# Optimization experiments

Hardware: AMD Instinct MI355X
Metric: run time of the kernel (lower is better)

The kernel has to match this reference:

```python
import jax, jax.numpy as jnp
import numpy as np

B, T = 16, 2048
V, E, H, C = 32000, 512, 4, 3  # vocab, embed, heads, context (history 2 + current)
EPS = 1e-5


def setup_inputs() -> dict:
    key = jax.random.key(0)
    k0, k1, k2, k3, k4, k5, k6 = jax.random.split(key, 7)
    tokens = jax.random.randint(k0, (B, T), 0, V)
    embed_table = jax.random.normal(k1, (V, E), dtype=jnp.float32)
    pos = jax.random.normal(k2, (H, E, C), dtype=jnp.float32) * (1.0 / np.sqrt(H))
    ffn_w = jax.random.normal(k3, (E, E), dtype=jnp.float32) * (1.0 / np.sqrt(E))
    ffn_b = jax.random.normal(k4, (E,), dtype=jnp.float32) * 0.01
    ln_g = jnp.ones((E,), dtype=jnp.float32)
    ln_b = jnp.zeros((E,), dtype=jnp.float32)
    return {"tokens": tokens, "embed_table": embed_table, "pos": pos,
            "ffn_w": ffn_w, "ffn_b": ffn_b, "ln_g": ln_g, "ln_b": ln_b}


def reference(tokens, embed_table, pos, ffn_w, ffn_b, ln_g, ln_b):
    # embed lookup: [B, T, E]
    x = embed_table[tokens]
    # prepend zero history, extract sliding windows of size C: [B, T, C, E]
    x_cat = jnp.concatenate([jnp.zeros((B, C - 1, E), dtype=x.dtype), x], axis=1)
    x_win = jnp.stack([x_cat[:, i:i + T] for i in range(C)], axis=2)
    # multi-head positional scores: pos viewed as [H, C, E]
    pos_hce = jnp.transpose(pos, (0, 2, 1))  # [H, C, E]
    w = jnp.einsum('btce,hce->bthc', x_win, pos_hce)          # scores
    out = jnp.einsum('bthc,btce->bte', w, x_win) / (H * C)    # weighted sum
    # FFN (torch Linear: y = x @ W^T + b)
    out = out @ ffn_w.T + ffn_b
    # LayerNorm
    mu = jnp.mean(out, axis=-1, keepdims=True)
    var = jnp.mean(jnp.square(out - mu), axis=-1, keepdims=True)
    out = (out - mu) * jax.lax.rsqrt(var + EPS) * ln_g + ln_b
    # swish
    return out * jax.nn.sigmoid(out)
```

## Files before the change

kernel.cpp:

```cpp
#include <hip/hip_runtime.h>
#include <hip/hip_bf16.h>


#define Bq 16
#define Tq 2048
#define Eq 512
#define Cq 3
#define Hq 4
#define Mq (Bq * Tq)
#define LN_EPS 1e-5f

typedef __attribute__((ext_vector_type(8))) short bf16x8;
typedef __attribute__((ext_vector_type(4))) float f32x4;
typedef __attribute__((ext_vector_type(8))) unsigned short u16x8;

__device__ __forceinline__ unsigned short f2bf(float f) {
    unsigned int u = __float_as_uint(f);
    u += 0x7fffu + ((u >> 16) & 1u);
    return (unsigned short)(u >> 16);
}

__global__ void prep_kernel(const float* __restrict__ pos,
                            const float* __restrict__ ffn_w,
                            float* __restrict__ Pt,
                            unsigned short* __restrict__ Wb) {
    int i = blockIdx.x * blockDim.x + threadIdx.x;
    if (i < Cq * Eq) {
        int c = i / Eq, e = i % Eq;
        float s = 0.f;
#pragma unroll
        for (int h = 0; h < Hq; ++h) s += pos[(h * Eq + e) * Cq + c];
        Pt[i] = s;
    }
    int nth = blockDim.x * gridDim.x;
    for (int j = i; j < Eq * Eq; j += nth) Wb[j] = f2bf(ffn_w[j]);
}

__global__ __launch_bounds__(256) void ctx_kernel(const int* __restrict__ tokens,
                                                  const float* __restrict__ tbl,
                                                  const float* __restrict__ Pt,
                                                  unsigned short* __restrict__ out1) {
    const int wave = threadIdx.x >> 6;
    const int lane = threadIdx.x & 63;
    const int tt = blockIdx.x * 4 + wave;
    const int b = tt >> 11;
    const int t = tt & (Tq - 1);

    float x[Cq][8];
    float s[Cq];
#pragma unroll
    for (int c = 0; c < Cq; ++c) {
        const int r = t - (Cq - 1) + c;
        if (r >= 0) {
            const int tok = tokens[(b << 11) + r];
            const float4* row = reinterpret_cast<const float4*>(tbl + (long)tok * Eq + lane * 8);
            float4 v0 = row[0], v1 = row[1];
            x[c][0] = v0.x; x[c][1] = v0.y; x[c][2] = v0.z; x[c][3] = v0.w;
            x[c][4] = v1.x; x[c][5] = v1.y; x[c][6] = v1.z; x[c][7] = v1.w;
        } else {
#pragma unroll
            for (int j = 0; j < 8; ++j) x[c][j] = 0.f;
        }
        const float4* pp = reinterpret_cast<const float4*>(Pt + c * Eq + lane * 8);
        float4 p0 = pp[0], p1 = pp[1];
        s[c] = x[c][0] * p0.x + x[c][1] * p0.y + x[c][2] * p0.z + x[c][3] * p0.w
             + x[c][4] * p1.x + x[c][5] * p1.y + x[c][6] * p1.z + x[c][7] * p1.w;
    }
#pragma unroll
    for (int m = 1; m < 64; m <<= 1) {
        s[0] += __shfl_xor(s[0], m, 64);
        s[1] += __shfl_xor(s[1], m, 64);
        s[2] += __shfl_xor(s[2], m, 64);
    }
    const float inv = 1.f / (Hq * Cq);
    u16x8 o;
#pragma unroll
    for (int j = 0; j < 8; ++j) {
        float v = (s[0] * x[0][j] + s[1] * x[1][j] + s[2] * x[2][j]) * inv;
        o[j] = f2bf(v);
    }
    *reinterpret_cast<u16x8*>(out1 + (long)tt * Eq + lane * 8) = o;
}

__global__ __launch_bounds__(512, 4) void ffn_ln_kernel(const unsigned short* __restrict__ A,
                                                        const unsigned short* __restrict__ Wb,
                                                        const float* __restrict__ bias,
                                                        const float* __restrict__ ln_g,
                                                        const float* __restrict__ ln_b,
                                                        float* __restrict__ out) {
    __shared__ __align__(16) char Atile[2][8192];
    __shared__ float lds_sum[64][8];
    __shared__ float lds_sq[64][8];
    __shared__ float lds_mu[64];
    __shared__ float lds_rs[64];

    const int tid = threadIdx.x;
    const int wave = tid >> 6;
    const int lane = tid & 63;
    const int lr = lane & 15;
    const int lg = lane >> 4;
    const int m0 = blockIdx.x << 6;
    const int n0 = wave << 6;

    const char* Ap = reinterpret_cast<const char*>(A) + (long)m0 * (Eq * 2);
    const short* Bp = reinterpret_cast<const short*>(Wb) + (long)n0 * Eq;

    const int r_st = tid >> 3;
    const int cb0 = (((tid & 7) ^ (r_st & 7)) << 4);
    const char* Asrc_base = Ap + r_st * 1024 + cb0;
    char* lds_wave_base[2];
    lds_wave_base[0] = &Atile[0][wave * 1024];
    lds_wave_base[1] = &Atile[1][wave * 1024];

    f32x4 acc[4][4];
#pragma unroll
    for (int i = 0; i < 4; ++i)
#pragma unroll
        for (int j = 0; j < 4; ++j) acc[i][j] = (f32x4){0.f, 0.f, 0.f, 0.f};

    __builtin_amdgcn_global_load_lds(
        (const __attribute__((address_space(1))) void*)(Asrc_base),
        (__attribute__((address_space(3))) void*)(lds_wave_base[0]), 16, 0, 0);
    __syncthreads();

    int buf = 0;
#pragma unroll
    for (int kb = 0; kb < 8; ++kb) {
        if (kb < 7) {
            __builtin_amdgcn_global_load_lds(
                (const __attribute__((address_space(1))) void*)(Asrc_base + (kb + 1) * 128),
                (__attribute__((address_space(3))) void*)(lds_wave_base[buf ^ 1]), 16, 0, 0);
        }
#pragma unroll
        for (int ks = 0; ks < 2; ++ks) {
            bf16x8 afrag[4], bfrag[4];
#pragma unroll
            for (int mf = 0; mf < 4; ++mf) {
                const int r = mf * 16 + lr;
                const int phys = r * 128 + ((ks * 64 + lg * 16) ^ ((r & 7) << 4));
                afrag[mf] = *reinterpret_cast<const bf16x8*>(&Atile[buf][phys]);
            }
#pragma unroll
            for (int nf = 0; nf < 4; ++nf)
                bfrag[nf] = *reinterpret_cast<const bf16x8*>(Bp + (nf * 16 + lr) * Eq + kb * 64 + ks * 32 + lg * 8);
#pragma unroll
            for (int mf = 0; mf < 4; ++mf)
#pragma unroll
                for (int nf = 0; nf < 4; ++nf)
                    acc[mf][nf] = __builtin_amdgcn_mfma_f32_16x16x32_bf16(afrag[mf], bfrag[nf], acc[mf][nf], 0, 0, 0);
        }
        __syncthreads();
        buf ^= 1;
    }

    float bcol[4];
#pragma unroll
    for (int nf = 0; nf < 4; ++nf) bcol[nf] = bias[n0 + nf * 16 + lr];

#pragma unroll
    for (int mf = 0; mf < 4; ++mf) {
#pragma unroll
        for (int i = 0; i < 4; ++i) {
            float sm = 0.f, sq = 0.f;
#pragma unroll
            for (int nf = 0; nf < 4; ++nf) {
                float v = acc[mf][nf][i] + bcol[nf];
                acc[mf][nf][i] = v;
                sm += v;
                sq += v * v;
            }
#pragma unroll
            for (int msk = 1; msk < 16; msk <<= 1) {
                sm += __shfl_xor(sm, msk, 64);
                sq += __shfl_xor(sq, msk, 64);
            }
            if (lr == 0) {
                const int row = mf * 16 + lg * 4 + i;
                lds_sum[row][wave] = sm;
                lds_sq[row][wave] = sq;
            }
        }
    }
    __syncthreads();
    if (tid < 64) {
        float sm = 0.f, sq = 0.f;
#pragma unroll
        for (int w = 0; w < 8; ++w) { sm += lds_sum[tid][w]; sq += lds_sq[tid][w]; }
        const float mu = sm * (1.f / Eq);
        const float var = sq * (1.f / Eq) - mu * mu;
        lds_mu[tid] = mu;
        lds_rs[tid] = rsqrtf(var + LN_EPS);
    }
    __syncthreads();

    float gcol[4], bbcol[4];
#pragma unroll
    for (int nf = 0; nf < 4; ++nf) {
        gcol[nf] = ln_g[n0 + nf * 16 + lr];
        bbcol[nf] = ln_b[n0 + nf * 16 + lr];
    }
#pragma unroll
    for (int mf = 0; mf < 4; ++mf) {
#pragma unroll
        for (int i = 0; i < 4; ++i) {
            const int row = mf * 16 + lg * 4 + i;
            const float mu = lds_mu[row];
            const float rs = lds_rs[row];
#pragma unroll
            for (int nf = 0; nf < 4; ++nf) {
                float v = acc[mf][nf][i];
                float o = (v - mu) * rs * gcol[nf] + bbcol[nf];
                o = o / (1.f + __expf(-o));
                out[(long)(m0 + row) * Eq + (n0 + nf * 16 + lr)] = o;
            }
        }
    }
}

extern "C" void kernel_launch(void* const* d_in, const int* in_sizes, int n_in,
                              void* d_out, int out_size, void* d_ws, size_t ws_size,
                              hipStream_t stream) {
    const int* tokens = (const int*)d_in[0];
    const float* tbl = (const float*)d_in[1];
    const float* pos = (const float*)d_in[2];
    const float* ffn_w = (const float*)d_in[3];
    const float* ffn_b = (const float*)d_in[4];
    const float* ln_g = (const float*)d_in[5];
    const float* ln_b = (const float*)d_in[6];
    float* out = (float*)d_out;

    char* ws = (char*)d_ws;
    float* Pt = (float*)ws;
    unsigned short* Wb = (unsigned short*)(ws + 8192);
    unsigned short* out1 = (unsigned short*)(ws + (1 << 20));

    hipLaunchKernelGGL(prep_kernel, dim3(64), dim3(256), 0, stream, pos, ffn_w, Pt, Wb);
    hipLaunchKernelGGL(ctx_kernel, dim3(Mq / 4), dim3(256), 0, stream, tokens, tbl, Pt, out1);
    hipLaunchKernelGGL(ffn_ln_kernel, dim3(Mq / 64), dim3(512), 0, stream, out1, Wb, ffn_b, ln_g, ln_b, out);
}
```

Before: 81.71 us.

## Fuse context-window gather into FFN+LayerNorm kernel with full LDS A tile

Merges the embedding gather and context-weighting kernel into the GEMM+LayerNorm kernel. Each wave gathers 10 embedding rows, reusing each across three windows instead of loading every row three times, and writes the bf16 activation row straight into a 64KB swizzled LDS tile. This removes the bf16 intermediate round-trip through global memory and one launch. The price is 64KB of LDS per block, which lowers occupancy below the declared launch bounds, plus a gather phase that no longer overlaps the MFMA loop. Embeddings are now rounded to bf16 before the weighted sum, a small precision change.

```diff
diff --git a/kernel.cpp b/kernel.cpp
--- a/kernel.cpp
+++ b/kernel.cpp
@@ -18,6 +18,9 @@
     unsigned int u = __float_as_uint(f);
     u += 0x7fffu + ((u >> 16) & 1u);
     return (unsigned short)(u >> 16);
+}
+__device__ __forceinline__ float bf2f(unsigned short h) {
+    return __uint_as_float(((unsigned int)h) << 16);
 }
 
 __global__ void prep_kernel(const float* __restrict__ pos,
@@ -36,59 +39,15 @@
     for (int j = i; j < Eq * Eq; j += nth) Wb[j] = f2bf(ffn_w[j]);
 }
 
-__global__ __launch_bounds__(256) void ctx_kernel(const int* __restrict__ tokens,
-                                                  const float* __restrict__ tbl,
-                                                  const float* __restrict__ Pt,
-                                                  unsigned short* __restrict__ out1) {
-    const int wave = threadIdx.x >> 6;
-    const int lane = threadIdx.x & 63;
-    const int tt = blockIdx.x * 4 + wave;
-    const int b = tt >> 11;
-    const int t = tt & (Tq - 1);
-
-    float x[Cq][8];
-    float s[Cq];
-#pragma unroll
-    for (int c = 0; c < Cq; ++c) {
-        const int r = t - (Cq - 1) + c;
-        if (r >= 0) {
-            const int tok = tokens[(b << 11) + r];
-            const float4* row = reinterpret_cast<const float4*>(tbl + (long)tok * Eq + lane * 8);
-            float4 v0 = row[0], v1 = row[1];
-            x[c][0] = v0.x; x[c][1] = v0.y; x[c][2] = v0.z; x[c][3] = v0.w;
-            x[c][4] = v1.x; x[c][5] = v1.y; x[c][6] = v1.z; x[c][7] = v1.w;
-        } else {
-#pragma unroll
-            for (int j = 0; j < 8; ++j) x[c][j] = 0.f;
-        }
-        const float4* pp = reinterpret_cast<const float4*>(Pt + c * Eq + lane * 8);
-        float4 p0 = pp[0], p1 = pp[1];
-        s[c] = x[c][0] * p0.x + x[c][1] * p0.y + x[c][2] * p0.z + x[c][3] * p0.w
-             + x[c][4] * p1.x + x[c][5] * p1.y + x[c][6] * p1.z + x[c][7] * p1.w;
-    }
-#pragma unroll
-    for (int m = 1; m < 64; m <<= 1) {
-        s[0] += __shfl_xor(s[0], m, 64);
-        s[1] += __shfl_xor(s[1], m, 64);
-        s[2] += __shfl_xor(s[2], m, 64);
-    }
-    const float inv = 1.f / (Hq * Cq);
-    u16x8 o;
-#pragma unroll
-    for (int j = 0; j < 8; ++j) {
-        float v = (s[0] * x[0][j] + s[1] * x[1][j] + s[2] * x[2][j]) * inv;
-        o[j] = f2bf(v);
-    }
-    *reinterpret_cast<u16x8*>(out1 + (long)tt * Eq + lane * 8) = o;
-}
-
-__global__ __launch_bounds__(512, 4) void ffn_ln_kernel(const unsigned short* __restrict__ A,
-                                                        const unsigned short* __restrict__ Wb,
-                                                        const float* __restrict__ bias,
-                                                        const float* __restrict__ ln_g,
-                                                        const float* __restrict__ ln_b,
-                                                        float* __restrict__ out) {
-    __shared__ __align__(16) char Atile[2][8192];
+__global__ __launch_bounds__(512, 4) void fused_kernel(const int* __restrict__ tokens,
+                                                       const float* __restrict__ tbl,
+                                                       const float* __restrict__ Pt,
+                                                       const unsigned short* __restrict__ Wb,
+                                                       const float* __restrict__ bias,
+                                                       const float* __restrict__ ln_g,
+                                                       const float* __restrict__ ln_b,
+                                                       float* __restrict__ out) {
+    __shared__ __align__(16) unsigned short Atile[64 * 512];
     __shared__ float lds_sum[64][8];
     __shared__ float lds_sq[64][8];
     __shared__ float lds_mu[64];
@@ -100,57 +59,95 @@
     const int lr = lane & 15;
     const int lg = lane >> 4;
     const int m0 = blockIdx.x << 6;
+    const int b = m0 >> 11;
+    const int t0w = (m0 & (Tq - 1)) + (wave << 3);
+
+    float4 pA[Cq], pB[Cq];
+#pragma unroll
+    for (int c = 0; c < Cq; ++c) {
+        const float4* pp = reinterpret_cast<const float4*>(Pt + c * Eq + lane * 8);
+        pA[c] = pp[0]; pB[c] = pp[1];
+    }
+
+    u16x8 xb[10];
+    float d[10][Cq];
+    const int tbase = b << 11;
+#pragma unroll
+    for (int li = 0; li < 10; ++li) {
+        const int t = t0w - 2 + li;
+        float4 v0 = {0.f, 0.f, 0.f, 0.f}, v1 = {0.f, 0.f, 0.f, 0.f};
+        if (t >= 0) {
+            const int tok = tokens[tbase + t];
+            const float4* rp = reinterpret_cast<const float4*>(tbl + (long)tok * Eq + lane * 8);
+            v0 = rp[0]; v1 = rp[1];
+        }
+#pragma unroll
+        for (int c = 0; c < Cq; ++c) {
+            d[li][c] = v0.x * pA[c].x + v0.y * pA[c].y + v0.z * pA[c].z + v0.w * pA[c].w
+                     + v1.x * pB[c].x + v1.y * pB[c].y + v1.z * pB[c].z + v1.w * pB[c].w;
+        }
+        u16x8 xv;
+        xv[0] = f2bf(v0.x); xv[1] = f2bf(v0.y); xv[2] = f2bf(v0.z); xv[3] = f2bf(v0.w);
+        xv[4] = f2bf(v1.x); xv[5] = f2bf(v1.y); xv[6] = f2bf(v1.z); xv[7] = f2bf(v1.w);
+        xb[li] = xv;
+    }
+#pragma unroll
+    for (int li = 0; li < 10; ++li) {
+#pragma unroll
+        for (int c = 0; c < Cq; ++c) {
+            if (li >= c && li - c <= 7) {
+#pragma unroll
+                for (int m = 1; m < 64; m <<= 1) d[li][c] += __shfl_xor(d[li][c], m, 64);
+            }
+        }
+    }
+    const float inv = 1.f / (Hq * Cq);
+#pragma unroll
+    for (int j = 0; j < 8; ++j) {
+        const float s0 = d[j][0] * inv, s1 = d[j + 1][1] * inv, s2 = d[j + 2][2] * inv;
+        u16x8 o;
+#pragma unroll
+        for (int e = 0; e < 8; ++e) {
+            const float a = s0 * bf2f((unsigned short)xb[j][e])
+                          + s1 * bf2f((unsigned short)xb[j + 1][e])
+                          + s2 * bf2f((unsigned short)xb[j + 2][e]);
+            o[e] = f2bf(a);
+        }
+        const int row = (wave << 3) + j;
+        const int phys = row * 1024 + ((lane * 16) ^ ((row & 7) << 4));
+        *reinterpret_cast<u16x8*>(reinterpret_cast<char*>(Atile) + phys) = o;
+    }
+    __syncthreads();
+
     const int n0 = wave << 6;
-
-    const char* Ap = reinterpret_cast<const char*>(A) + (long)m0 * (Eq * 2);
     const short* Bp = reinterpret_cast<const short*>(Wb) + (long)n0 * Eq;
 
-    const int r_st = tid >> 3;
-    const int cb0 = (((tid & 7) ^ (r_st & 7)) << 4);
-    const char* Asrc_base = Ap + r_st * 1024 + cb0;
-    char* lds_wave_base[2];
-    lds_wave_base[0] = &Atile[0][wave * 1024];
-    lds_wave_base[1] = &Atile[1][wave * 1024];
-
     f32x4 acc[4][4];
 #pragma unroll
     for (int i = 0; i < 4; ++i)
 #pragma unroll
         for (int j = 0; j < 4; ++j) acc[i][j] = (f32x4){0.f, 0.f, 0.f, 0.f};
 
-    __builtin_amdgcn_global_load_lds(
-        (const __attribute__((address_space(1))) void*)(Asrc_base),
-        (__attribute__((address_space(3))) void*)(lds_wave_base[0]), 16, 0, 0);
-    __syncthreads();
-
-    int buf = 0;
 #pragma unroll
     for (int kb = 0; kb < 8; ++kb) {
-        if (kb < 7) {
-            __builtin_amdgcn_global_load_lds(
-                (const __attribute__((address_space(1))) void*)(Asrc_base + (kb + 1) * 128),
-                (__attribute__((address_space(3))) void*)(lds_wave_base[buf ^ 1]), 16, 0, 0);
-        }
 #pragma unroll
         for (int ks = 0; ks < 2; ++ks) {
-            bf16x8 afrag[4], bfrag[4];
+            bf16x8 af[4], bfv[4];
 #pragma unroll
             for (int mf = 0; mf < 4; ++mf) {
                 const int r = mf * 16 + lr;
-                const int phys = r * 128 + ((ks * 64 + lg * 16) ^ ((r & 7) << 4));
-                afrag[mf] = *reinterpret_cast<const bf16x8*>(&Atile[buf][phys]);
+                const int phys = r * 1024 + ((kb * 128 + ks * 64 + lg * 16) ^ ((r & 7) << 4));
+                af[mf] = *reinterpret_cast<const bf16x8*>(reinterpret_cast<const char*>(Atile) + phys);
             }
 #pragma unroll
             for (int nf = 0; nf < 4; ++nf)
-                bfrag[nf] = *reinterpret_cast<const bf16x8*>(Bp + (nf * 16 + lr) * Eq + kb * 64 + ks * 32 + lg * 8);
+                bfv[nf] = *reinterpret_cast<const bf16x8*>(Bp + (nf * 16 + lr) * Eq + kb * 64 + ks * 32 + lg * 8);
 #pragma unroll
             for (int mf = 0; mf < 4; ++mf)
 #pragma unroll
                 for (int nf = 0; nf < 4; ++nf)
-                    acc[mf][nf] = __builtin_amdgcn_mfma_f32_16x16x32_bf16(afrag[mf], bfrag[nf], acc[mf][nf], 0, 0, 0);
-        }
-        __syncthreads();
-        buf ^= 1;
+                    acc[mf][nf] = __builtin_amdgcn_mfma_f32_16x16x32_bf16(af[mf], bfv[nf], acc[mf][nf], 0, 0, 0);
+        }
     }
 
     float bcol[4];
@@ -232,9 +229,8 @@
     char* ws = (char*)d_ws;
     float* Pt = (float*)ws;
     unsigned short* Wb = (unsigned short*)(ws + 8192);
-    unsigned short* out1 = (unsigned short*)(ws + (1 << 20));
 
     hipLaunchKernelGGL(prep_kernel, dim3(64), dim3(256), 0, stream, pos, ffn_w, Pt, Wb);
-    hipLaunchKernelGGL(ctx_kernel, dim3(Mq / 4), dim3(256), 0, stream, tokens, tbl, Pt, out1);
-    hipLaunchKernelGGL(ffn_ln_kernel, dim3(Mq / 64), dim3(512), 0, stream, out1, Wb, ffn_b, ln_g, ln_b, out);
-}
+    hipLaunchKernelGGL(fused_kernel, dim3(Mq / 64), dim3(512), 0, stream,
+                       tokens, tbl, Pt, Wb, ffn_b, ln_g, ln_b, out);
+}
```

Measured after the change: 74.80 us. -8.5%, faster.

## Pre-swizzle intermediate layout and stage full A tile plus pipelined W in LDS

Applied to the files above, without the earlier changes.

The context kernel now writes its bf16 output directly in a per-64-row swizzled tile layout, using packed hardware bf16 conversion. The FFN kernel loads the whole 64x512 A tile into LDS at once and streams per-wave W slices through a double-buffered LDS pipeline with explicit waitcnt. Previously W fragments were read straight from global memory. This is meant to cut global-load latency on W and to drop the per-step block barriers, at the cost of 128KB+ of LDS, which forces lower occupancy (launch bounds 2).

```diff
diff --git a/kernel.cpp b/kernel.cpp
--- a/kernel.cpp
+++ b/kernel.cpp
@@ -12,12 +12,19 @@
 
 typedef __attribute__((ext_vector_type(8))) short bf16x8;
 typedef __attribute__((ext_vector_type(4))) float f32x4;
-typedef __attribute__((ext_vector_type(8))) unsigned short u16x8;
-
+
+__device__ __forceinline__ unsigned int cvt_pk_bf16(float lo, float hi) {
+    unsigned int r;
+    asm("v_cvt_pk_bf16_f32 %0, %1, %2" : "=v"(r) : "v"(lo), "v"(hi));
+    return r;
+}
 __device__ __forceinline__ unsigned short f2bf(float f) {
     unsigned int u = __float_as_uint(f);
     u += 0x7fffu + ((u >> 16) & 1u);
     return (unsigned short)(u >> 16);
+}
+__device__ __forceinline__ int xaddr(int row, int kbyte) {
+    return row * 1024 + (kbyte ^ ((row & 7) << 4));
 }
 
 __global__ void prep_kernel(const float* __restrict__ pos,
@@ -39,7 +46,7 @@
 __global__ __launch_bounds__(256) void ctx_kernel(const int* __restrict__ tokens,
                                                   const float* __restrict__ tbl,
                                                   const float* __restrict__ Pt,
-                                                  unsigned short* __restrict__ out1) {
+                                                  char* __restrict__ out1) {
     const int wave = threadIdx.x >> 6;
     const int lane = threadIdx.x & 63;
     const int tt = blockIdx.x * 4 + wave;
@@ -73,24 +80,29 @@
         s[2] += __shfl_xor(s[2], m, 64);
     }
     const float inv = 1.f / (Hq * Cq);
-    u16x8 o;
-#pragma unroll
-    for (int j = 0; j < 8; ++j) {
-        float v = (s[0] * x[0][j] + s[1] * x[1][j] + s[2] * x[2][j]) * inv;
-        o[j] = f2bf(v);
-    }
-    *reinterpret_cast<u16x8*>(out1 + (long)tt * Eq + lane * 8) = o;
-}
-
-__global__ __launch_bounds__(512, 4) void ffn_ln_kernel(const unsigned short* __restrict__ A,
-                                                        const unsigned short* __restrict__ Wb,
-                                                        const float* __restrict__ bias,
-                                                        const float* __restrict__ ln_g,
-                                                        const float* __restrict__ ln_b,
-                                                        float* __restrict__ out) {
-    __shared__ __align__(16) char Atile[2][8192];
-    __shared__ float lds_sum[64][8];
-    __shared__ float lds_sq[64][8];
+    float a[8];
+#pragma unroll
+    for (int j = 0; j < 8; ++j)
+        a[j] = (s[0] * x[0][j] + s[1] * x[1][j] + s[2] * x[2][j]) * inv;
+    uint4 o;
+    o.x = cvt_pk_bf16(a[0], a[1]);
+    o.y = cvt_pk_bf16(a[2], a[3]);
+    o.z = cvt_pk_bf16(a[4], a[5]);
+    o.w = cvt_pk_bf16(a[6], a[7]);
+    char* dst = out1 + ((long)(tt >> 6) << 16) + xaddr(tt & 63, lane * 16);
+    *reinterpret_cast<uint4*>(dst) = o;
+}
+
+__global__ __launch_bounds__(512, 2) void ffn_kernel(const char* __restrict__ A1,
+                                                     const unsigned short* __restrict__ Wb,
+                                                     const float* __restrict__ bias,
+                                                     const float* __restrict__ ln_g,
+                                                     const float* __restrict__ ln_b,
+                                                     float* __restrict__ out) {
+    __shared__ __align__(16) char Alds[65536];
+    __shared__ __align__(16) char Blds[65536];
+    __shared__ float Sm[64][8];
+    __shared__ float Sq[64][8];
     __shared__ float lds_mu[64];
     __shared__ float lds_rs[64];
 
@@ -102,15 +114,33 @@
     const int m0 = blockIdx.x << 6;
     const int n0 = wave << 6;
 
-    const char* Ap = reinterpret_cast<const char*>(A) + (long)m0 * (Eq * 2);
-    const short* Bp = reinterpret_cast<const short*>(Wb) + (long)n0 * Eq;
-
-    const int r_st = tid >> 3;
-    const int cb0 = (((tid & 7) ^ (r_st & 7)) << 4);
-    const char* Asrc_base = Ap + r_st * 1024 + cb0;
-    char* lds_wave_base[2];
-    lds_wave_base[0] = &Atile[0][wave * 1024];
-    lds_wave_base[1] = &Atile[1][wave * 1024];
+    const char* Asrc = A1 + ((long)blockIdx.x << 16);
+    const char* WbB = reinterpret_cast<const char*>(Wb);
+    char* Bw = Blds + wave * 8192;
+
+    const int rn_base = lane >> 2;
+    const int s_slot = lane & 3;
+
+#pragma unroll
+    for (int q = 0; q < 8; ++q) {
+        __builtin_amdgcn_global_load_lds(
+            (const __attribute__((address_space(1))) void*)(Asrc + wave * 8192 + q * 1024 + lane * 16),
+            (__attribute__((address_space(3))) void*)(Alds + wave * 8192 + q * 1024), 16, 0, 0);
+    }
+#pragma unroll
+    for (int kc0 = 0; kc0 < 2; ++kc0) {
+#pragma unroll
+        for (int q = 0; q < 4; ++q) {
+            const int rn = q * 16 + rn_base;
+            const int n = n0 + rn;
+            const int gb = n * 1024 + kc0 * 64 + ((s_slot * 16) ^ ((n & 3) << 4));
+            __builtin_amdgcn_global_load_lds(
+                (const __attribute__((address_space(1))) void*)(WbB + gb),
+                (__attribute__((address_space(3))) void*)(Bw + kc0 * 4096 + q * 1024), 16, 0, 0);
+        }
+    }
+    asm volatile("s_waitcnt vmcnt(8)" ::: "memory");
+    __syncthreads();
 
     f32x4 acc[4][4];
 #pragma unroll
@@ -118,39 +148,38 @@
 #pragma unroll
         for (int j = 0; j < 4; ++j) acc[i][j] = (f32x4){0.f, 0.f, 0.f, 0.f};
 
-    __builtin_amdgcn_global_load_lds(
-        (const __attribute__((address_space(1))) void*)(Asrc_base),
-        (__attribute__((address_space(3))) void*)(lds_wave_base[0]), 16, 0, 0);
-    __syncthreads();
-
-    int buf = 0;
-#pragma unroll
-    for (int kb = 0; kb < 8; ++kb) {
-        if (kb < 7) {
-            __builtin_amdgcn_global_load_lds(
-                (const __attribute__((address_space(1))) void*)(Asrc_base + (kb + 1) * 128),
-                (__attribute__((address_space(3))) void*)(lds_wave_base[buf ^ 1]), 16, 0, 0);
-        }
-#pragma unroll
-        for (int ks = 0; ks < 2; ++ks) {
-            bf16x8 afrag[4], bfrag[4];
-#pragma unroll
-            for (int mf = 0; mf < 4; ++mf) {
-                const int r = mf * 16 + lr;
-                const int phys = r * 128 + ((ks * 64 + lg * 16) ^ ((r & 7) << 4));
-                afrag[mf] = *reinterpret_cast<const bf16x8*>(&Atile[buf][phys]);
-            }
+#pragma unroll
+    for (int kc = 0; kc < 16; ++kc) {
+        const int buf = (kc & 1) * 4096;
+        bf16x8 af[4], bfv[4];
+#pragma unroll
+        for (int mf = 0; mf < 4; ++mf)
+            af[mf] = *reinterpret_cast<const bf16x8*>(Alds + xaddr(mf * 16 + lr, kc * 64 + lg * 16));
+#pragma unroll
+        for (int nf = 0; nf < 4; ++nf) {
+            const int rn = nf * 16 + lr;
+            bfv[nf] = *reinterpret_cast<const bf16x8*>(Bw + buf + rn * 64 + ((lg * 16) ^ ((rn & 3) << 4)));
+        }
+        if (kc < 14) {
+            asm volatile("s_waitcnt lgkmcnt(0)" ::: "memory");
+            const int kn = kc + 2;
+#pragma unroll
+            for (int q = 0; q < 4; ++q) {
+                const int rn = q * 16 + rn_base;
+                const int n = n0 + rn;
+                const int gb = n * 1024 + kn * 64 + ((s_slot * 16) ^ ((n & 3) << 4));
+                __builtin_amdgcn_global_load_lds(
+                    (const __attribute__((address_space(1))) void*)(WbB + gb),
+                    (__attribute__((address_space(3))) void*)(Bw + buf + q * 1024), 16, 0, 0);
+            }
+        }
+#pragma unroll
+        for (int mf = 0; mf < 4; ++mf)
 #pragma unroll
             for (int nf = 0; nf < 4; ++nf)
-                bfrag[nf] = *reinterpret_cast<const bf16x8*>(Bp + (nf * 16 + lr) * Eq + kb * 64 + ks * 32 + lg * 8);
-#pragma unroll
-            for (int mf = 0; mf < 4; ++mf)
-#pragma unroll
-                for (int nf = 0; nf < 4; ++nf)
-                    acc[mf][nf] = __builtin_amdgcn_mfma_f32_16x16x32_bf16(afrag[mf], bfrag[nf], acc[mf][nf], 0, 0, 0);
-        }
-        __syncthreads();
-        buf ^= 1;
+                acc[mf][nf] = __builtin_amdgcn_mfma_f32_16x16x32_bf16(af[mf], bfv[nf], acc[mf][nf], 0, 0, 0);
+        if (kc < 14)       asm volatile("s_waitcnt vmcnt(4)" ::: "memory");
+        else if (kc == 14) asm volatile("s_waitcnt vmcnt(0)" ::: "memory");
     }
 
     float bcol[4];
@@ -175,9 +204,9 @@
                 sq += __shfl_xor(sq, msk, 64);
             }
             if (lr == 0) {
-                const int row = mf * 16 + lg * 4 + i;
-                lds_sum[row][wave] = sm;
-                lds_sq[row][wave] = sq;
+                const int row = mf * 16 + (lg << 2) + i;
+                Sm[row][wave] = sm;
+                Sq[row][wave] = sq;
             }
         }
     }
@@ -185,7 +214,7 @@
     if (tid < 64) {
         float sm = 0.f, sq = 0.f;
 #pragma unroll
-        for (int w = 0; w < 8; ++w) { sm += lds_sum[tid][w]; sq += lds_sq[tid][w]; }
+        for (int w = 0; w < 8; ++w) { sm += Sm[tid][w]; sq += Sq[tid][w]; }
         const float mu = sm * (1.f / Eq);
         const float var = sq * (1.f / Eq) - mu * mu;
         lds_mu[tid] = mu;
@@ -203,7 +232,7 @@
     for (int mf = 0; mf < 4; ++mf) {
 #pragma unroll
         for (int i = 0; i < 4; ++i) {
-            const int row = mf * 16 + lg * 4 + i;
+            const int row = mf * 16 + (lg << 2) + i;
             const float mu = lds_mu[row];
             const float rs = lds_rs[row];
 #pragma unroll
@@ -232,9 +261,10 @@
     char* ws = (char*)d_ws;
     float* Pt = (float*)ws;
     unsigned short* Wb = (unsigned short*)(ws + 8192);
-    unsigned short* out1 = (unsigned short*)(ws + (1 << 20));
+    char* out1 = ws + (1 << 20);
 
     hipLaunchKernelGGL(prep_kernel, dim3(64), dim3(256), 0, stream, pos, ffn_w, Pt, Wb);
     hipLaunchKernelGGL(ctx_kernel, dim3(Mq / 4), dim3(256), 0, stream, tokens, tbl, Pt, out1);
-    hipLaunchKernelGGL(ffn_ln_kernel, dim3(Mq / 64), dim3(512), 0, stream, out1, Wb, ffn_b, ln_g, ln_b, out);
-}
+    hipLaunchKernelGGL(ffn_kernel, dim3(Mq / 64), dim3(512), 0, stream,
+                       out1, Wb, ffn_b, ln_g, ln_b, out);
+}
```

Measured after the change: 75.22 us. 7.9% less time.
